# Performance work log

Hardware: AMD Instinct MI355X
Metric: run time of the kernel (lower is better)

The kernel has to match this reference:

```python
import jax, jax.numpy as jnp
import numpy as np

BS, N, D_IN, D_OUT = 4, 512, 64, 64
TEMP = 1.0
POOL_K = 0.5
N_KEEP = max(int(N * POOL_K), 1)  # 256
BN_EPS = 1e-5


def setup_inputs() -> dict:
    key = jax.random.key(0)
    ks = jax.random.split(key, 12)
    xav = lambda k, shape: jax.random.normal(k, shape, jnp.float32) * np.sqrt(2.0 / sum(shape))
    return {
        "x": jax.random.normal(ks[0], (BS, N, D_IN), jnp.float32),
        "att_proj_w": xav(ks[1], (D_IN, D_OUT)),
        "att_proj_b": jnp.zeros((D_OUT,), jnp.float32),
        "att_weight": xav(ks[2], (D_OUT, 1))[:, 0],  # (D_OUT,)
        "pwa_w": xav(ks[3], (D_IN, D_OUT)),
        "pwa_b": jnp.zeros((D_OUT,), jnp.float32),
        "pwoa_w": xav(ks[4], (D_IN, D_OUT)),
        "pwoa_b": jnp.zeros((D_OUT,), jnp.float32),
        "bn_gamma": jnp.ones((D_OUT,), jnp.float32),
        "bn_beta": jnp.zeros((D_OUT,), jnp.float32),
        "bn_mean": jnp.zeros((D_OUT,), jnp.float32),
        "bn_var": jnp.ones((D_OUT,), jnp.float32),
        "pool_w": xav(ks[5], (D_OUT, 1))[:, 0],  # (D_OUT,)
        "pool_b": jnp.zeros((), jnp.float32),
    }


def reference(x, att_proj_w, att_proj_b, att_weight, pwa_w, pwa_b,
              pwoa_w, pwoa_b, bn_gamma, bn_beta, bn_mean, bn_var,
              pool_w, pool_b):
    # ---- GraphAttentionLayer (eval mode: dropout off, BN uses running stats) ----
    # pairwise node product: (bs, i, j, d)
    pair = x[:, :, None, :] * x[:, None, :, :]
    a = jnp.tanh(jnp.einsum('bijd,de->bije', pair, att_proj_w) + att_proj_b)
    scores = jnp.einsum('bije,e->bij', a, att_weight) / TEMP
    att = jax.nn.softmax(scores, axis=-1)  # torch softmax over dim=-2 of (bs,i,j,1) == j axis
    agg = jnp.einsum('bij,bjd->bid', att, x)
    h = (agg @ pwa_w + pwa_b) + (x @ pwoa_w + pwoa_b)
    h = (h - bn_mean) * jax.lax.rsqrt(bn_var + BN_EPS) * bn_gamma + bn_beta
    h = jax.nn.selu(h)
    # ---- GraphPool (eval: dropout off) ----
    s = jax.nn.sigmoid(h @ pool_w + pool_b)  # (bs, N)
    _, idx = jax.lax.top_k(s, N_KEEP)        # (bs, N_KEEP), sorted desc like torch.topk
    hs = h * s[..., None]
    out = jnp.take_along_axis(hs, idx[..., None], axis=1)  # (bs, N_KEEP, D_OUT)
    return out
```

## Files before the change

### kernel.cpp

```cpp
#include <hip/hip_runtime.h>
#include <hip/hip_bf16.h>
#include <math.h>

#define BSZ 4
#define NN 512
#define DD 64
#define NKEEP 256

typedef __attribute__((ext_vector_type(8))) short short8;
typedef __attribute__((ext_vector_type(4))) float f32x4;

__device__ __forceinline__ ushort f2bf_rne(float f) {
  union { float f; unsigned u; } v; v.f = f;
  unsigned r = v.u + 0x7fffu + ((v.u >> 16) & 1u);
  return (ushort)(r >> 16);
}
__device__ __forceinline__ float bf2f(ushort h) {
  union { unsigned u; float f; } v; v.u = ((unsigned)h) << 16;
  return v.f;
}
__device__ __forceinline__ float fast_tanh(float x) {
  float e = __builtin_amdgcn_exp2f(x * 2.8853900817779268f);
  float r = __builtin_amdgcn_rcpf(e + 1.0f);
  return 1.0f - 2.0f * r;
}

__global__ __launch_bounds__(256, 2) void k_score(
    const float* __restrict__ x, const float* __restrict__ apw,
    const float* __restrict__ apb, const float* __restrict__ aw,
    float* __restrict__ sTp) {
  __shared__ float Xi_s[16 * 64];
  __shared__ ushort Yh[2][4 * 16 * 64];
  __shared__ ushort Yl[2][4 * 16 * 64];

  const int t = threadIdx.x;
  const int w = t >> 6, l = t & 63;
  const int b = blockIdx.x / 160;
  const int rem = blockIdx.x % 160;
  const int eh = rem / 80;
  const int tid = rem % 80;
  int jq, it;
  if (tid < 8)        { jq = 0; it = tid; }
  else if (tid < 24)  { jq = 1; it = tid - 8; }
  else if (tid < 48)  { jq = 2; it = tid - 24; }
  else                { jq = 3; it = tid - 48; }
  const int i0 = it * 16;
  const int jb0 = jq * 128;
  const int eh32 = eh * 32;
  const bool fast = (jb0 >= i0 + 16);

  const float* xb = x + (size_t)b * NN * DD;
  const int j0 = jb0 + w * 32;
  const bool wave_active = (j0 + 32 > i0);

  {
    const int row = t >> 4, dq = (t & 15) * 4;
    *reinterpret_cast<float4*>(&Xi_s[row * 64 + dq]) =
        *reinterpret_cast<const float4*>(xb + (size_t)(i0 + row) * DD + dq);
  }

  short8 ah[2][2], al[2][2];
  if (wave_active) {
    const int g = l >> 4;
    #pragma unroll
    for (int jt = 0; jt < 2; ++jt) {
      const int j = j0 + jt * 16 + (l & 15);
      #pragma unroll
      for (int ks = 0; ks < 2; ++ks) {
        const float* xr = xb + (size_t)j * DD + ks * 32 + g * 8;
        float4 u0 = *reinterpret_cast<const float4*>(xr);
        float4 u1 = *reinterpret_cast<const float4*>(xr + 4);
        float vv[8] = {u0.x, u0.y, u0.z, u0.w, u1.x, u1.y, u1.z, u1.w};
        short8 hh, ll;
        #pragma unroll
        for (int qq = 0; qq < 8; ++qq) {
          ushort hq = f2bf_rne(vv[qq]);
          hh[qq] = (short)hq;
          ll[qq] = (short)f2bf_rne(vv[qq] - bf2f(hq));
        }
        ah[jt][ks] = hh; al[jt][ks] = ll;
      }
    }
  }

  const int bi_g = l >> 4;
  const int bdq = (l & 15) * 4;
  auto build = [&](int rnd, int bf) {
    const int e = eh32 + rnd * 4 + w;
    float wt[4];
    #pragma unroll
    for (int k = 0; k < 4; ++k) wt[k] = apw[(bdq + k) * 64 + e];
    #pragma unroll
    for (int i2 = 0; i2 < 4; ++i2) {
      const int i = i2 * 4 + bi_g;
      float4 xv = *reinterpret_cast<const float4*>(&Xi_s[i * 64 + bdq]);
      const float p0v = xv.x * wt[0], p1v = xv.y * wt[1];
      const float p2v = xv.z * wt[2], p3v = xv.w * wt[3];
      const ushort h0 = f2bf_rne(p0v), h1 = f2bf_rne(p1v);
      const ushort h2 = f2bf_rne(p2v), h3 = f2bf_rne(p3v);
      uint2 hw, lw;
      hw.x = (uint)h0 | ((uint)h1 << 16);
      hw.y = (uint)h2 | ((uint)h3 << 16);
      lw.x = (uint)f2bf_rne(p0v - bf2f(h0)) | ((uint)f2bf_rne(p1v - bf2f(h1)) << 16);
      lw.y = (uint)f2bf_rne(p2v - bf2f(h2)) | ((uint)f2bf_rne(p3v - bf2f(h3)) << 16);
      const int byteoff = (w * 2048 + (i * 64 + bdq) * 2) ^ ((i & 7) << 4);
      *reinterpret_cast<uint2*>(reinterpret_cast<char*>(Yh[bf]) + byteoff) = hw;
      *reinterpret_cast<uint2*>(reinterpret_cast<char*>(Yl[bf]) + byteoff) = lw;
    }
  };

  const int il = l & 15, g = l >> 4;
  const int fbyte0 = ((il * 64 + g * 8) * 2) ^ ((il & 7) << 4);
  const int fbyte1 = ((il * 64 + 32 + g * 8) * 2) ^ ((il & 7) << 4);

  f32x4 srews[2];
  srews[0] = (f32x4){0.f, 0.f, 0.f, 0.f};
  srews[1] = (f32x4){0.f, 0.f, 0.f, 0.f};

  __syncthreads();
  build(0, 0);

  #pragma unroll 1
  for (int r = 0; r < 8; ++r) {
    __syncthreads();
    const char* Ph = reinterpret_cast<const char*>(Yh[r & 1]);
    const char* Pl = reinterpret_cast<const char*>(Yl[r & 1]);

    short8 cbh0, cbh1, cbl0, cbl1;
    if (wave_active) {
      cbh0 = *reinterpret_cast<const short8*>(Ph + fbyte0);
      cbh1 = *reinterpret_cast<const short8*>(Ph + fbyte1);
      cbl0 = *reinterpret_cast<const short8*>(Pl + fbyte0);
      cbl1 = *reinterpret_cast<const short8*>(Pl + fbyte1);
    }
    if (r < 7) build(r + 1, (r + 1) & 1);

    if (wave_active) {
      #pragma unroll
      for (int p = 0; p < 4; ++p) {
        short8 nbh0, nbh1, nbl0, nbl1;
        if (p < 3) {
          nbh0 = *reinterpret_cast<const short8*>(Ph + (p + 1) * 2048 + fbyte0);
          nbh1 = *reinterpret_cast<const short8*>(Ph + (p + 1) * 2048 + fbyte1);
          nbl0 = *reinterpret_cast<const short8*>(Pl + (p + 1) * 2048 + fbyte0);
          nbl1 = *reinterpret_cast<const short8*>(Pl + (p + 1) * 2048 + fbyte1);
        }
        f32x4 a00 = (f32x4){0.f, 0.f, 0.f, 0.f};
        f32x4 a01 = (f32x4){0.f, 0.f, 0.f, 0.f};
        f32x4 a10 = (f32x4){0.f, 0.f, 0.f, 0.f};
        f32x4 a11 = (f32x4){0.f, 0.f, 0.f, 0.f};
        a00 = __builtin_amdgcn_mfma_f32_16x16x32_bf16(ah[0][0], cbh0, a00, 0, 0, 0);
        a10 = __builtin_amdgcn_mfma_f32_16x16x32_bf16(ah[1][0], cbh0, a10, 0, 0, 0);
        a01 = __builtin_amdgcn_mfma_f32_16x16x32_bf16(ah[0][1], cbh1, a01, 0, 0, 0);
        a11 = __builtin_amdgcn_mfma_f32_16x16x32_bf16(ah[1][1], cbh1, a11, 0, 0, 0);
        a00 = __builtin_amdgcn_mfma_f32_16x16x32_bf16(ah[0][0], cbl0, a00, 0, 0, 0);
        a10 = __builtin_amdgcn_mfma_f32_16x16x32_bf16(ah[1][0], cbl0, a10, 0, 0, 0);
        a01 = __builtin_amdgcn_mfma_f32_16x16x32_bf16(ah[0][1], cbl1, a01, 0, 0, 0);
        a11 = __builtin_amdgcn_mfma_f32_16x16x32_bf16(ah[1][1], cbl1, a11, 0, 0, 0);
        a00 = __builtin_amdgcn_mfma_f32_16x16x32_bf16(al[0][0], cbh0, a00, 0, 0, 0);
        a10 = __builtin_amdgcn_mfma_f32_16x16x32_bf16(al[1][0], cbh0, a10, 0, 0, 0);
        a01 = __builtin_amdgcn_mfma_f32_16x16x32_bf16(al[0][1], cbh1, a01, 0, 0, 0);
        a11 = __builtin_amdgcn_mfma_f32_16x16x32_bf16(al[1][1], cbh1, a11, 0, 0, 0);

        const int e = eh32 + r * 4 + p;
        const float bias = apb[e], awv = aw[e];
        #pragma unroll
        for (int rr = 0; rr < 4; ++rr) {
          srews[0][rr] += awv * fast_tanh(a00[rr] + a01[rr] + bias);
          srews[1][rr] += awv * fast_tanh(a10[rr] + a11[rr] + bias);
        }
        cbh0 = nbh0; cbh1 = nbh1; cbl0 = nbl0; cbl1 = nbl1;
      }
    }
  }

  float* plane = sTp + ((size_t)(eh * 4 + b)) * NN * NN;
  const int iv = i0 + il;
  if (fast) {
    #pragma unroll
    for (int jt = 0; jt < 2; ++jt)
      #pragma unroll
      for (int rr = 0; rr < 4; ++rr)
        plane[(size_t)(j0 + jt * 16 + g * 4 + rr) * NN + iv] = srews[jt][rr];
    __syncthreads();
    float* T = reinterpret_cast<float*>(Yh[0]);
    #pragma unroll
    for (int jt = 0; jt < 2; ++jt)
      #pragma unroll
      for (int rr = 0; rr < 4; ++rr) {
        const int colw = w * 32 + jt * 16 + g * 4 + rr;
        const int byteoff = ((il * 128 + colw) * 4) ^ ((il & 7) << 4);
        *reinterpret_cast<float*>(reinterpret_cast<char*>(T) + byteoff) =
            srews[jt][rr];
      }
    __syncthreads();
    const int row = t >> 4, cb = (t & 15) * 8;
    const char* Tc = reinterpret_cast<const char*>(T);
    const int base = (row * 128 + cb) * 4;
    const int sw = (row & 7) << 4;
    f32x4 v0 = *reinterpret_cast<const f32x4*>(Tc + ((base) ^ sw));
    f32x4 v1 = *reinterpret_cast<const f32x4*>(Tc + ((base + 16) ^ sw));
    *reinterpret_cast<f32x4*>(plane + (size_t)(i0 + row) * NN + jb0 + cb) = v0;
    *reinterpret_cast<f32x4*>(plane + (size_t)(i0 + row) * NN + jb0 + cb + 4) = v1;
  } else if (wave_active) {
    #pragma unroll
    for (int jt = 0; jt < 2; ++jt)
      #pragma unroll
      for (int rr = 0; rr < 4; ++rr) {
        const int jv = j0 + jt * 16 + g * 4 + rr;
        const float v = srews[jt][rr];
        if (jv >= iv) plane[(size_t)iv * NN + jv] = v;
        if (jv > iv) plane[(size_t)jv * NN + iv] = v;
      }
  }
}

__global__ __launch_bounds__(256) void k_soft(
    const float* __restrict__ x, const float* __restrict__ sTp,
    const float* __restrict__ pwa, const float* __restrict__ pwab,
    const float* __restrict__ pwoa, const float* __restrict__ pwob,
    const float* __restrict__ gam, const float* __restrict__ bet,
    const float* __restrict__ mu, const float* __restrict__ var,
    const float* __restrict__ poolw, const float* __restrict__ poolb,
    float* __restrict__ h, float* __restrict__ s) {
  __shared__ float ssc[2][512];
  __shared__ float srm[2][4], srs[2][4];
  __shared__ float sagg[4][2][64];
  __shared__ float rag[2][64], xis[2][64];

  const int t = threadIdx.x;
  const int w = t >> 6, l = t & 63;
  const int b = blockIdx.x >> 8;
  const int rp = blockIdx.x & 255;
  const int i_r0 = rp * 2, i_r1 = i_r0 + 1;
  const float* xb = x + (size_t)b * NN * DD;
  const float* pl0 = sTp + (size_t)b * NN * NN;
  const float* pl1 = sTp + (size_t)(4 + b) * NN * NN;
  const int jw = w * 128;

  const size_t o0 = (size_t)i_r0 * NN + jw + l;
  const size_t o1 = (size_t)i_r1 * NN + jw + l;
  float r0a = pl0[o0] + pl1[o0];
  float r0b = pl0[o0 + 64] + pl1[o0 + 64];
  float r1a = pl0[o1] + pl1[o1];
  float r1b = pl0[o1 + 64] + pl1[o1 + 64];
  float m0 = fmaxf(r0a, r0b), m1 = fmaxf(r1a, r1b);
  #pragma unroll
  for (int off = 32; off; off >>= 1) {
    m0 = fmaxf(m0, __shfl_xor(m0, off, 64));
    m1 = fmaxf(m1, __shfl_xor(m1, off, 64));
  }
  if (l == 0) { srm[0][w] = m0; srm[1][w] = m1; }
  __syncthreads();
  m0 = fmaxf(fmaxf(srm[0][0], srm[0][1]), fmaxf(srm[0][2], srm[0][3]));
  m1 = fmaxf(fmaxf(srm[1][0], srm[1][1]), fmaxf(srm[1][2], srm[1][3]));

  const float L2E = 1.4426950408889634f;
  float e0a = __builtin_amdgcn_exp2f((r0a - m0) * L2E);
  float e0b = __builtin_amdgcn_exp2f((r0b - m0) * L2E);
  float e1a = __builtin_amdgcn_exp2f((r1a - m1) * L2E);
  float e1b = __builtin_amdgcn_exp2f((r1b - m1) * L2E);
  float ps0 = e0a + e0b, ps1 = e1a + e1b;
  #pragma unroll
  for (int off = 32; off; off >>= 1) {
    ps0 += __shfl_xor(ps0, off, 64);
    ps1 += __shfl_xor(ps1, off, 64);
  }
  if (l == 0) { srs[0][w] = ps0; srs[1][w] = ps1; }
  __syncthreads();
  const float inv0 = 1.f / (srs[0][0] + srs[0][1] + srs[0][2] + srs[0][3]);
  const float inv1 = 1.f / (srs[1][0] + srs[1][1] + srs[1][2] + srs[1][3]);
  ssc[0][jw + l] = e0a * inv0;
  ssc[0][jw + 64 + l] = e0b * inv0;
  ssc[1][jw + l] = e1a * inv1;
  ssc[1][jw + 64 + l] = e1b * inv1;
  __syncthreads();

  float g0a = 0.f, g0b = 0.f, g1a = 0.f, g1b = 0.f;
  #pragma unroll 4
  for (int jj = 0; jj < 128; jj += 2) {
    const int j = jw + jj;
    const float xv0 = xb[(size_t)j * DD + l];
    const float xv1 = xb[(size_t)(j + 1) * DD + l];
    g0a = fmaf(ssc[0][j], xv0, g0a);
    g1a = fmaf(ssc[1][j], xv0, g1a);
    g0b = fmaf(ssc[0][j + 1], xv1, g0b);
    g1b = fmaf(ssc[1][j + 1], xv1, g1b);
  }
  sagg[w][0][l] = g0a + g0b;
  sagg[w][1][l] = g1a + g1b;
  __syncthreads();

  if (w < 2) {
    const int irow = i_r0 + w;
    rag[w][l] = sagg[0][w][l] + sagg[1][w][l] + sagg[2][w][l] + sagg[3][w][l];
    xis[w][l] = xb[(size_t)irow * DD + l];
    float acc = 0.f;
    #pragma unroll 8
    for (int d = 0; d < 64; ++d) {
      acc = fmaf(rag[w][d], pwa[d * 64 + l], acc);
      acc = fmaf(xis[w][d], pwoa[d * 64 + l], acc);
    }
    acc += pwab[l] + pwob[l];
    float hb = (acc - mu[l]) * rsqrtf(var[l] + 1e-5f) * gam[l] + bet[l];
    const float SC = 1.0507009873554805f, AL = 1.6732632423543772f;
    float hv = hb > 0.f ? SC * hb : SC * AL * expm1f(hb);
    h[((size_t)(b * NN + irow)) * DD + l] = hv;

    float p = hv * poolw[l];
    #pragma unroll
    for (int off = 32; off; off >>= 1) p += __shfl_xor(p, off, 64);
    if (l == 0) s[b * NN + irow] = 1.f / (1.f + expf(-(p + poolb[0])));
  }
}

__global__ __launch_bounds__(512) void k_topk(
    const float* __restrict__ s, int* __restrict__ invi,
    float* __restrict__ sval) {
  __shared__ float sv[NN];
  const int b = blockIdx.x, t = threadIdx.x;
  sv[t] = s[b * NN + t];
  __syncthreads();

  const float my = sv[t];
  int r = 0;
  #pragma unroll 4
  for (int j0 = 0; j0 < NN; j0 += 4) {
    float4 v = *reinterpret_cast<const float4*>(&sv[j0]);
    r += (v.x > my) || (v.x == my && (j0 + 0) < t);
    r += (v.y > my) || (v.y == my && (j0 + 1) < t);
    r += (v.z > my) || (v.z == my && (j0 + 2) < t);
    r += (v.w > my) || (v.w == my && (j0 + 3) < t);
  }
  if (r < NKEEP) { invi[b * NKEEP + r] = t; sval[b * NKEEP + r] = my; }
}

__global__ __launch_bounds__(256) void k_gather(
    const int* __restrict__ invi, const float* __restrict__ sval,
    const float* __restrict__ h, float* __restrict__ out) {
  const int b = blockIdx.x >> 4, kg = blockIdx.x & 15;
  const int t = threadIdx.x;
  const int kk = kg * 16 + (t >> 4);
  const int d4 = (t & 15) * 4;
  const int i = invi[b * NKEEP + kk];
  const float svv = sval[b * NKEEP + kk];
  float4 v = *reinterpret_cast<const float4*>(h + ((size_t)(b * NN + i)) * DD + d4);
  v.x *= svv; v.y *= svv; v.z *= svv; v.w *= svv;
  *reinterpret_cast<float4*>(out + ((size_t)(b * NKEEP + kk)) * DD + d4) = v;
}

extern "C" void kernel_launch(void* const* d_in, const int* in_sizes, int n_in,
                              void* d_out, int out_size, void* d_ws, size_t ws_size,
                              hipStream_t stream) {
  const float* x     = (const float*)d_in[0];
  const float* apw   = (const float*)d_in[1];
  const float* apb   = (const float*)d_in[2];
  const float* aw    = (const float*)d_in[3];
  const float* pwa   = (const float*)d_in[4];
  const float* pwab  = (const float*)d_in[5];
  const float* pwoa  = (const float*)d_in[6];
  const float* pwob  = (const float*)d_in[7];
  const float* gam   = (const float*)d_in[8];
  const float* bet   = (const float*)d_in[9];
  const float* mu    = (const float*)d_in[10];
  const float* var   = (const float*)d_in[11];
  const float* poolw = (const float*)d_in[12];
  const float* poolb = (const float*)d_in[13];
  float* out = (float*)d_out;

  float* sTp = (float*)d_ws;
  float* h   = sTp + (size_t)2 * BSZ * NN * NN;
  float* s   = h + (size_t)BSZ * NN * DD;
  int* invi  = (int*)(s + BSZ * NN);
  float* sval = (float*)(invi + BSZ * NKEEP);

  k_score<<<640, 256, 0, stream>>>(x, apw, apb, aw, sTp);
  k_soft<<<BSZ * 256, 256, 0, stream>>>(x, sTp, pwa, pwab, pwoa, pwob,
                                        gam, bet, mu, var, poolw, poolb, h, s);
  k_topk<<<BSZ, 512, 0, stream>>>(s, invi, sval);
  k_gather<<<BSZ * 16, 256, 0, stream>>>(invi, sval, h, out);
}
```

Measured before the change: 70.34 us.

## Shrink score tiles, simplify tanh accumulation, fuse topk with gather

The score kernel now gives each wave one 16-column j-tile instead of two, so each block covers 64 columns and the grid grows from 640 to 1152 blocks. That gives finer triangular work balance and lower register pressure. The per-block shared-memory copy of the i-rows is dropped, and build reads them straight from global memory. The tanh weighting is folded algebraically into sum(aw) minus 2*aw*rcp(exp+1), which saves an operation per element. The topk and gather kernels are merged into a single launch that keeps the indices in shared memory, trading one launch for a gather parallelised over only 4 blocks.

Result: no change. 71.26 us (+1.3%).

```diff
diff --git a/kernel.cpp b/kernel.cpp
--- a/kernel.cpp
+++ b/kernel.cpp
@@ -19,69 +19,67 @@
   union { unsigned u; float f; } v; v.u = ((unsigned)h) << 16;
   return v.f;
 }
-__device__ __forceinline__ float fast_tanh(float x) {
-  float e = __builtin_amdgcn_exp2f(x * 2.8853900817779268f);
-  float r = __builtin_amdgcn_rcpf(e + 1.0f);
-  return 1.0f - 2.0f * r;
-}
 
 __global__ __launch_bounds__(256, 2) void k_score(
     const float* __restrict__ x, const float* __restrict__ apw,
     const float* __restrict__ apb, const float* __restrict__ aw,
     float* __restrict__ sTp) {
-  __shared__ float Xi_s[16 * 64];
   __shared__ ushort Yh[2][4 * 16 * 64];
   __shared__ ushort Yl[2][4 * 16 * 64];
 
   const int t = threadIdx.x;
   const int w = t >> 6, l = t & 63;
-  const int b = blockIdx.x / 160;
-  const int rem = blockIdx.x % 160;
-  const int eh = rem / 80;
-  const int tid = rem % 80;
-  int jq, it;
-  if (tid < 8)        { jq = 0; it = tid; }
-  else if (tid < 24)  { jq = 1; it = tid - 8; }
-  else if (tid < 48)  { jq = 2; it = tid - 24; }
-  else                { jq = 3; it = tid - 48; }
+  const int bid = blockIdx.x;
+  const int b = bid / 288;
+  const int rem = bid % 288;
+  const int eh = rem / 144;
+  const int tid = rem % 144;
+  int m, base;
+  if (tid < 40) {
+    if (tid < 4)        { m = 0; base = 0; }
+    else if (tid < 12)  { m = 1; base = 4; }
+    else if (tid < 24)  { m = 2; base = 12; }
+    else                { m = 3; base = 24; }
+  } else {
+    if (tid < 60)       { m = 4; base = 40; }
+    else if (tid < 84)  { m = 5; base = 60; }
+    else if (tid < 112) { m = 6; base = 84; }
+    else                { m = 7; base = 112; }
+  }
+  const int it = tid - base;
   const int i0 = it * 16;
-  const int jb0 = jq * 128;
+  const int jb0 = m * 64;
   const int eh32 = eh * 32;
   const bool fast = (jb0 >= i0 + 16);
 
   const float* xb = x + (size_t)b * NN * DD;
-  const int j0 = jb0 + w * 32;
-  const bool wave_active = (j0 + 32 > i0);
-
-  {
-    const int row = t >> 4, dq = (t & 15) * 4;
-    *reinterpret_cast<float4*>(&Xi_s[row * 64 + dq]) =
-        *reinterpret_cast<const float4*>(xb + (size_t)(i0 + row) * DD + dq);
-  }
-
-  short8 ah[2][2], al[2][2];
+  const int j0 = jb0 + w * 16;
+  const bool wave_active = (j0 + 16 > i0);
+
+  short8 ah[2], al[2];
   if (wave_active) {
     const int g = l >> 4;
-    #pragma unroll
-    for (int jt = 0; jt < 2; ++jt) {
-      const int j = j0 + jt * 16 + (l & 15);
+    const int j = j0 + (l & 15);
+    #pragma unroll
+    for (int ks = 0; ks < 2; ++ks) {
+      const float* xr = xb + (size_t)j * DD + ks * 32 + g * 8;
+      float4 u0 = *reinterpret_cast<const float4*>(xr);
+      float4 u1 = *reinterpret_cast<const float4*>(xr + 4);
+      float vv[8] = {u0.x, u0.y, u0.z, u0.w, u1.x, u1.y, u1.z, u1.w};
+      short8 hh, ll;
       #pragma unroll
-      for (int ks = 0; ks < 2; ++ks) {
-        const float* xr = xb + (size_t)j * DD + ks * 32 + g * 8;
-        float4 u0 = *reinterpret_cast<const float4*>(xr);
-        float4 u1 = *reinterpret_cast<const float4*>(xr + 4);
-        float vv[8] = {u0.x, u0.y, u0.z, u0.w, u1.x, u1.y, u1.z, u1.w};
-        short8 hh, ll;
-        #pragma unroll
-        for (int qq = 0; qq < 8; ++qq) {
-          ushort hq = f2bf_rne(vv[qq]);
-          hh[qq] = (short)hq;
-          ll[qq] = (short)f2bf_rne(vv[qq] - bf2f(hq));
-        }
-        ah[jt][ks] = hh; al[jt][ks] = ll;
+      for (int qq = 0; qq < 8; ++qq) {
+        ushort hq = f2bf_rne(vv[qq]);
+        hh[qq] = (short)hq;
+        ll[qq] = (short)f2bf_rne(vv[qq] - bf2f(hq));
       }
-    }
-  }
+      ah[ks] = hh; al[ks] = ll;
+    }
+  }
+
+  float awC = 0.f;
+  #pragma unroll 8
+  for (int e = 0; e < 32; ++e) awC += aw[eh32 + e];
 
   const int bi_g = l >> 4;
   const int bdq = (l & 15) * 4;
@@ -93,7 +91,8 @@
     #pragma unroll
     for (int i2 = 0; i2 < 4; ++i2) {
       const int i = i2 * 4 + bi_g;
-      float4 xv = *reinterpret_cast<const float4*>(&Xi_s[i * 64 + bdq]);
+      float4 xv = *reinterpret_cast<const float4*>(
+          xb + (size_t)(i0 + i) * DD + bdq);
       const float p0v = xv.x * wt[0], p1v = xv.y * wt[1];
       const float p2v = xv.z * wt[2], p3v = xv.w * wt[3];
       const ushort h0 = f2bf_rne(p0v), h1 = f2bf_rne(p1v);
@@ -112,12 +111,10 @@
   const int il = l & 15, g = l >> 4;
   const int fbyte0 = ((il * 64 + g * 8) * 2) ^ ((il & 7) << 4);
   const int fbyte1 = ((il * 64 + 32 + g * 8) * 2) ^ ((il & 7) << 4);
-
-  f32x4 srews[2];
-  srews[0] = (f32x4){0.f, 0.f, 0.f, 0.f};
-  srews[1] = (f32x4){0.f, 0.f, 0.f, 0.f};
-
-  __syncthreads();
+  const float K2 = 2.8853900817779268f;
+
+  f32x4 srews = (f32x4){0.f, 0.f, 0.f, 0.f};
+
   build(0, 0);
 
   #pragma unroll 1
@@ -145,73 +142,61 @@
           nbl0 = *reinterpret_cast<const short8*>(Pl + (p + 1) * 2048 + fbyte0);
           nbl1 = *reinterpret_cast<const short8*>(Pl + (p + 1) * 2048 + fbyte1);
         }
-        f32x4 a00 = (f32x4){0.f, 0.f, 0.f, 0.f};
-        f32x4 a01 = (f32x4){0.f, 0.f, 0.f, 0.f};
-        f32x4 a10 = (f32x4){0.f, 0.f, 0.f, 0.f};
-        f32x4 a11 = (f32x4){0.f, 0.f, 0.f, 0.f};
-        a00 = __builtin_amdgcn_mfma_f32_16x16x32_bf16(ah[0][0], cbh0, a00, 0, 0, 0);
-        a10 = __builtin_amdgcn_mfma_f32_16x16x32_bf16(ah[1][0], cbh0, a10, 0, 0, 0);
-        a01 = __builtin_amdgcn_mfma_f32_16x16x32_bf16(ah[0][1], cbh1, a01, 0, 0, 0);
-        a11 = __builtin_amdgcn_mfma_f32_16x16x32_bf16(ah[1][1], cbh1, a11, 0, 0, 0);
-        a00 = __builtin_amdgcn_mfma_f32_16x16x32_bf16(ah[0][0], cbl0, a00, 0, 0, 0);
-        a10 = __builtin_amdgcn_mfma_f32_16x16x32_bf16(ah[1][0], cbl0, a10, 0, 0, 0);
-        a01 = __builtin_amdgcn_mfma_f32_16x16x32_bf16(ah[0][1], cbl1, a01, 0, 0, 0);
-        a11 = __builtin_amdgcn_mfma_f32_16x16x32_bf16(ah[1][1], cbl1, a11, 0, 0, 0);
-        a00 = __builtin_amdgcn_mfma_f32_16x16x32_bf16(al[0][0], cbh0, a00, 0, 0, 0);
-        a10 = __builtin_amdgcn_mfma_f32_16x16x32_bf16(al[1][0], cbh0, a10, 0, 0, 0);
-        a01 = __builtin_amdgcn_mfma_f32_16x16x32_bf16(al[0][1], cbh1, a01, 0, 0, 0);
-        a11 = __builtin_amdgcn_mfma_f32_16x16x32_bf16(al[1][1], cbh1, a11, 0, 0, 0);
+        f32x4 a0 = (f32x4){0.f, 0.f, 0.f, 0.f};
+        f32x4 a1 = (f32x4){0.f, 0.f, 0.f, 0.f};
+        a0 = __builtin_amdgcn_mfma_f32_16x16x32_bf16(ah[0], cbh0, a0, 0, 0, 0);
+        a1 = __builtin_amdgcn_mfma_f32_16x16x32_bf16(ah[1], cbh1, a1, 0, 0, 0);
+        a0 = __builtin_amdgcn_mfma_f32_16x16x32_bf16(ah[0], cbl0, a0, 0, 0, 0);
+        a1 = __builtin_amdgcn_mfma_f32_16x16x32_bf16(ah[1], cbl1, a1, 0, 0, 0);
+        a0 = __builtin_amdgcn_mfma_f32_16x16x32_bf16(al[0], cbh0, a0, 0, 0, 0);
+        a1 = __builtin_amdgcn_mfma_f32_16x16x32_bf16(al[1], cbh1, a1, 0, 0, 0);
 
         const int e = eh32 + r * 4 + p;
-        const float bias = apb[e], awv = aw[e];
+        const float bias = apb[e];
+        const float aw2 = 2.f * aw[e];
         #pragma unroll
         for (int rr = 0; rr < 4; ++rr) {
-          srews[0][rr] += awv * fast_tanh(a00[rr] + a01[rr] + bias);
-          srews[1][rr] += awv * fast_tanh(a10[rr] + a11[rr] + bias);
+          const float vv = a0[rr] + a1[rr] + bias;
+          const float ex = __builtin_amdgcn_exp2f(vv * K2);
+          const float rc = __builtin_amdgcn_rcpf(ex + 1.0f);
+          srews[rr] = fmaf(-aw2, rc, srews[rr]);
         }
         cbh0 = nbh0; cbh1 = nbh1; cbl0 = nbl0; cbl1 = nbl1;
       }
     }
   }
 
+  f32x4 sv4;
+  #pragma unroll
+  for (int rr = 0; rr < 4; ++rr) sv4[rr] = srews[rr] + awC;
+
   float* plane = sTp + ((size_t)(eh * 4 + b)) * NN * NN;
   const int iv = i0 + il;
   if (fast) {
     #pragma unroll
-    for (int jt = 0; jt < 2; ++jt)
-      #pragma unroll
-      for (int rr = 0; rr < 4; ++rr)
-        plane[(size_t)(j0 + jt * 16 + g * 4 + rr) * NN + iv] = srews[jt][rr];
+    for (int rr = 0; rr < 4; ++rr)
+      plane[(size_t)(j0 + g * 4 + rr) * NN + iv] = sv4[rr];
     __syncthreads();
     float* T = reinterpret_cast<float*>(Yh[0]);
-    #pragma unroll
-    for (int jt = 0; jt < 2; ++jt)
-      #pragma unroll
-      for (int rr = 0; rr < 4; ++rr) {
-        const int colw = w * 32 + jt * 16 + g * 4 + rr;
-        const int byteoff = ((il * 128 + colw) * 4) ^ ((il & 7) << 4);
-        *reinterpret_cast<float*>(reinterpret_cast<char*>(T) + byteoff) =
-            srews[jt][rr];
-      }
+    {
+      const int byteoff = ((il * 64 + w * 16 + g * 4) * 4) ^ ((il & 7) << 4);
+      *reinterpret_cast<f32x4*>(reinterpret_cast<char*>(T) + byteoff) = sv4;
+    }
     __syncthreads();
-    const int row = t >> 4, cb = (t & 15) * 8;
-    const char* Tc = reinterpret_cast<const char*>(T);
-    const int base = (row * 128 + cb) * 4;
-    const int sw = (row & 7) << 4;
-    f32x4 v0 = *reinterpret_cast<const f32x4*>(Tc + ((base) ^ sw));
-    f32x4 v1 = *reinterpret_cast<const f32x4*>(Tc + ((base + 16) ^ sw));
-    *reinterpret_cast<f32x4*>(plane + (size_t)(i0 + row) * NN + jb0 + cb) = v0;
-    *reinterpret_cast<f32x4*>(plane + (size_t)(i0 + row) * NN + jb0 + cb + 4) = v1;
+    {
+      const int row = t >> 4, cb4 = (t & 15) * 4;
+      const int byteoff = ((row * 64 + cb4) * 4) ^ ((row & 7) << 4);
+      f32x4 v = *reinterpret_cast<const f32x4*>(
+          reinterpret_cast<const char*>(T) + byteoff);
+      *reinterpret_cast<f32x4*>(plane + (size_t)(i0 + row) * NN + jb0 + cb4) = v;
+    }
   } else if (wave_active) {
     #pragma unroll
-    for (int jt = 0; jt < 2; ++jt)
-      #pragma unroll
-      for (int rr = 0; rr < 4; ++rr) {
-        const int jv = j0 + jt * 16 + g * 4 + rr;
-        const float v = srews[jt][rr];
-        if (jv >= iv) plane[(size_t)iv * NN + jv] = v;
-        if (jv > iv) plane[(size_t)jv * NN + iv] = v;
-      }
+    for (int rr = 0; rr < 4; ++rr) {
+      const int jv = j0 + g * 4 + rr;
+      if (jv >= iv) plane[(size_t)iv * NN + jv] = sv4[rr];
+      if (jv > iv) plane[(size_t)jv * NN + iv] = sv4[rr];
+    }
   }
 }
 
@@ -314,39 +299,39 @@
   }
 }
 
-__global__ __launch_bounds__(512) void k_topk(
-    const float* __restrict__ s, int* __restrict__ invi,
-    float* __restrict__ sval) {
-  __shared__ float sv[NN];
+__global__ __launch_bounds__(512) void k_sel(
+    const float* __restrict__ s, const float* __restrict__ h,
+    float* __restrict__ out) {
+  __shared__ float svv[NN];
+  __shared__ int inv[NKEEP];
+  __shared__ float sval[NKEEP];
   const int b = blockIdx.x, t = threadIdx.x;
-  sv[t] = s[b * NN + t];
-  __syncthreads();
-
-  const float my = sv[t];
+  svv[t] = s[b * NN + t];
+  __syncthreads();
+
+  const float my = svv[t];
   int r = 0;
   #pragma unroll 4
   for (int j0 = 0; j0 < NN; j0 += 4) {
-    float4 v = *reinterpret_cast<const float4*>(&sv[j0]);
+    float4 v = *reinterpret_cast<const float4*>(&svv[j0]);
     r += (v.x > my) || (v.x == my && (j0 + 0) < t);
     r += (v.y > my) || (v.y == my && (j0 + 1) < t);
     r += (v.z > my) || (v.z == my && (j0 + 2) < t);
     r += (v.w > my) || (v.w == my && (j0 + 3) < t);
   }
-  if (r < NKEEP) { invi[b * NKEEP + r] = t; sval[b * NKEEP + r] = my; }
-}
-
-__global__ __launch_bounds__(256) void k_gather(
-    const int* __restrict__ invi, const float* __restrict__ sval,
-    const float* __restrict__ h, float* __restrict__ out) {
-  const int b = blockIdx.x >> 4, kg = blockIdx.x & 15;
-  const int t = threadIdx.x;
-  const int kk = kg * 16 + (t >> 4);
-  const int d4 = (t & 15) * 4;
-  const int i = invi[b * NKEEP + kk];
-  const float svv = sval[b * NKEEP + kk];
-  float4 v = *reinterpret_cast<const float4*>(h + ((size_t)(b * NN + i)) * DD + d4);
-  v.x *= svv; v.y *= svv; v.z *= svv; v.w *= svv;
-  *reinterpret_cast<float4*>(out + ((size_t)(b * NKEEP + kk)) * DD + d4) = v;
+  if (r < NKEEP) { inv[r] = t; sval[r] = my; }
+  __syncthreads();
+
+  #pragma unroll
+  for (int pos = t; pos < NKEEP * 16; pos += 512) {
+    const int kk = pos >> 4, d4 = (pos & 15) * 4;
+    const int i = inv[kk];
+    const float sc = sval[kk];
+    float4 v = *reinterpret_cast<const float4*>(
+        h + ((size_t)(b * NN + i)) * DD + d4);
+    v.x *= sc; v.y *= sc; v.z *= sc; v.w *= sc;
+    *reinterpret_cast<float4*>(out + ((size_t)(b * NKEEP + kk)) * DD + d4) = v;
+  }
 }
 
 extern "C" void kernel_launch(void* const* d_in, const int* in_sizes, int n_in,
@@ -371,12 +356,9 @@
   float* sTp = (float*)d_ws;
   float* h   = sTp + (size_t)2 * BSZ * NN * NN;
   float* s   = h + (size_t)BSZ * NN * DD;
-  int* invi  = (int*)(s + BSZ * NN);
-  float* sval = (float*)(invi + BSZ * NKEEP);
-
-  k_score<<<640, 256, 0, stream>>>(x, apw, apb, aw, sTp);
+
+  k_score<<<1152, 256, 0, stream>>>(x, apw, apb, aw, sTp);
   k_soft<<<BSZ * 256, 256, 0, stream>>>(x, sTp, pwa, pwab, pwoa, pwob,
                                         gam, bet, mu, var, poolw, poolb, h, s);
-  k_topk<<<BSZ, 512, 0, stream>>>(s, invi, sval);
-  k_gather<<<BSZ * 16, 256, 0, stream>>>(invi, sval, h, out);
-}
+  k_sel<<<BSZ, 512, 0, stream>>>(s, h, out);
+}
```
